# Performance work log

Measured on AMD Instinct MI355X. Metric: run time of the kernel, lower is better.

## Reference

```python
import jax, jax.numpy as jnp
import numpy as np

N_NODES = 10000
N_EDGES = 200000
NODE_DIM = 128
EDGE_DIM = 16
CONV_DIM = 64
HEADS = 5
NEG_SLOPE = 0.2


def gatv2_layer(x, src, dst, edge_attr, Wl, bl, We, att, bias):
    # PyG GATv2Conv, share_weights=True, concat=False, add_self_loops=True, eval mode
    N = x.shape[0]
    H, C = att.shape
    xl = (x @ Wl + bl).reshape(N, H, C)  # [N,H,C]; x_r = x_l (share_weights)
    # self loops, edge_attr fill_value='mean' (mean of incoming edge_attr per node)
    deg = jax.ops.segment_sum(jnp.ones(dst.shape[0], x.dtype), dst, num_segments=N)
    loop_attr = jax.ops.segment_sum(edge_attr, dst, num_segments=N) / jnp.maximum(deg, 1.0)[:, None]
    loop = jnp.arange(N, dtype=src.dtype)
    src_f = jnp.concatenate([src, loop])
    dst_f = jnp.concatenate([dst, loop])
    ea = jnp.concatenate([edge_attr, loop_attr], axis=0)
    e_emb = (ea @ We).reshape(-1, H, C)  # [E+N,H,C]
    m = jax.nn.leaky_relu(xl[src_f] + xl[dst_f] + e_emb, NEG_SLOPE)
    score = jnp.einsum('ehc,hc->eh', m, att)  # [E+N,H]
    # per-destination softmax over incoming edges
    smax = jax.ops.segment_max(score, dst_f, num_segments=N)
    ex = jnp.exp(score - smax[dst_f])
    denom = jax.ops.segment_sum(ex, dst_f, num_segments=N)
    alpha = ex / denom[dst_f]
    out = jax.ops.segment_sum(alpha[:, :, None] * xl[src_f], dst_f, num_segments=N)
    return out.mean(axis=1) + bias  # concat=False -> mean over heads


def setup_inputs() -> dict:
    key = jax.random.key(0)
    ks = jax.random.split(key, 32)
    inp = {
        'x': jax.random.normal(ks[0], (N_NODES, NODE_DIM), jnp.float32),
        'edge_index': jax.random.randint(ks[1], (2, N_EDGES), 0, N_NODES, dtype=jnp.int32),
        'edge_attr': jax.random.normal(ks[2], (N_EDGES, EDGE_DIM), jnp.float32),
    }
    in_dims = [NODE_DIM, CONV_DIM, CONV_DIM]
    HC = HEADS * CONV_DIM
    k = 3
    for l in range(3):
        d = in_dims[l]
        inp[f'Wl{l}'] = jax.random.normal(ks[k], (d, HC), jnp.float32) / np.float32(np.sqrt(d)); k += 1
        inp[f'bl{l}'] = jnp.zeros((HC,), jnp.float32)
        inp[f'We{l}'] = jax.random.normal(ks[k], (EDGE_DIM, HC), jnp.float32) / np.float32(np.sqrt(EDGE_DIM)); k += 1
        inp[f'att{l}'] = jax.random.normal(ks[k], (HEADS, CONV_DIM), jnp.float32) / np.float32(np.sqrt(CONV_DIM)); k += 1
        inp[f'b{l}'] = jnp.zeros((CONV_DIM,), jnp.float32)
    return inp


def reference(x, edge_index, edge_attr,
              Wl0, bl0, We0, att0, b0,
              Wl1, bl1, We1, att1, b1,
              Wl2, bl2, We2, att2, b2):
    src, dst = edge_index[0], edge_index[1]
    h = x
    layers = [(Wl0, bl0, We0, att0, b0), (Wl1, bl1, We1, att1, b1), (Wl2, bl2, We2, att2, b2)]
    for Wl, bl, We, att, b in layers:
        h = gatv2_layer(h, src, dst, edge_attr, Wl, bl, We, att, b)
        h = jax.nn.elu(h)
    return h
```

## Files before the change

### kernel.cpp

```cpp
#include <hip/hip_runtime.h>
#include <hip/hip_bf16.h>


#define NN 10000
#define NE 200000
#define ND 128
#define ED 16
#define CD 64
#define NH 5
#define HC 320
#define EF 210000
#define EFP 210048
#define NEG 0.2f
#define SB 103

__global__ void k_count(const int* __restrict__ dst, int* __restrict__ deg) {
  int e = blockIdx.x * blockDim.x + threadIdx.x;
  if (e >= NE) return;
  atomicAdd(&deg[dst[e]], 1);
}

__global__ __launch_bounds__(1024) void k_scan(const int* __restrict__ deg,
                                               int* __restrict__ rowptr) {
  __shared__ int part[1024];
  int t = threadIdx.x;
  int base = t * 10;
  int local[10];
  int s = 0;
  #pragma unroll
  for (int j = 0; j < 10; j++) {
    int i = base + j;
    local[j] = (i < NN) ? deg[i] : 0;
    s += local[j];
  }
  part[t] = s;
  __syncthreads();
  for (int off = 1; off < 1024; off <<= 1) {
    int v = (t >= off) ? part[t - off] : 0;
    __syncthreads();
    part[t] += v;
    __syncthreads();
  }
  int prefix = (t > 0) ? part[t - 1] : 0;
  #pragma unroll
  for (int j = 0; j < 10; j++) {
    int i = base + j;
    if (i < NN) rowptr[i] = prefix;
    prefix += local[j];
  }
  if (t == 1023) rowptr[NN] = prefix;
}

__global__ void k_fill(const int* __restrict__ ei, const int* __restrict__ rowptr,
                       int* __restrict__ cursor, int* __restrict__ csr_eid,
                       int* __restrict__ csr_src, int* __restrict__ csr_dst) {
  int e = blockIdx.x * blockDim.x + threadIdx.x;
  if (e >= NE) return;
  int d = ei[NE + e];
  int slot = atomicAdd(&cursor[d], 1);
  int pos = rowptr[d] + slot;
  csr_eid[pos] = e;
  csr_src[pos] = ei[e];
  csr_dst[pos] = d;
}

__global__ __launch_bounds__(256) void k_loopattr(const int* __restrict__ csr_eid,
                                                  const int* __restrict__ rowptr,
                                                  const float* __restrict__ eattr,
                                                  float* __restrict__ loop_attr) {
  int wave = threadIdx.x >> 6, lane = threadIdx.x & 63;
  int d = blockIdx.x * 4 + wave;
  if (d >= NN) return;
  int g = lane >> 4, k = lane & 15;
  int b = rowptr[d], n = rowptr[d + 1] - b;
  float s = 0.f;
  for (int i = g; i < n; i += 4)
    s += eattr[(size_t)csr_eid[b + i] * ED + k];
  s += __shfl_xor(s, 16, 64);
  s += __shfl_xor(s, 32, 64);
  if (g == 0) loop_attr[d * ED + k] = s / fmaxf((float)n, 1.0f);
}

__global__ void k_eacsr(const int* __restrict__ csr_eid, const float* __restrict__ eattr,
                        float* __restrict__ ea_csr) {
  int idx = blockIdx.x * blockDim.x + threadIdx.x;
  if (idx >= NE * 4) return;
  int p = idx >> 2, q = idx & 3;
  const float4* sp = (const float4*)(eattr + (size_t)csr_eid[p] * ED);
  ((float4*)(ea_csr + (size_t)p * ED))[q] = sp[q];
}

__global__ void k_wet(const float* __restrict__ We, float* __restrict__ WeT) {
  int i = blockIdx.x * blockDim.x + threadIdx.x;
  if (i >= ED * HC) return;
  int hc = i >> 4, k = i & 15;
  WeT[i] = We[k * HC + hc];
}

template <int D>
__global__ __launch_bounds__(320) void k_xl(const float* __restrict__ h,
                                            const float* __restrict__ Wl,
                                            const float* __restrict__ bl,
                                            float* __restrict__ xl) {
  constexpr int NPB = 8;
  int node0 = blockIdx.x * NPB;
  int t = threadIdx.x;
  float acc[NPB];
  #pragma unroll
  for (int i = 0; i < NPB; i++) acc[i] = 0.f;
  for (int k = 0; k < D; k += 4) {
    float w0 = Wl[(k + 0) * HC + t];
    float w1 = Wl[(k + 1) * HC + t];
    float w2 = Wl[(k + 2) * HC + t];
    float w3 = Wl[(k + 3) * HC + t];
    #pragma unroll
    for (int i = 0; i < NPB; i++) {
      float4 hv = *(const float4*)(h + (size_t)(node0 + i) * D + k);
      acc[i] += hv.x * w0 + hv.y * w1 + hv.z * w2 + hv.w * w3;
    }
  }
  float bv = bl[t];
  #pragma unroll
  for (int i = 0; i < NPB; i++)
    xl[(size_t)(node0 + i) * HC + t] = acc[i] + bv;
}

__device__ __forceinline__ float dot4(float4 a, float4 b) {
  return a.x * b.x + a.y * b.y + a.z * b.z + a.w * b.w;
}

__global__ __launch_bounds__(256) void k_score(
    const int* __restrict__ csr_src, const int* __restrict__ csr_dst,
    const float* __restrict__ ea_csr, const float* __restrict__ loop_attr,
    const float* __restrict__ xl, const float* __restrict__ WeT,
    const float* __restrict__ att, float* __restrict__ wP) {
  int bid = blockIdx.x;
  int lb = (bid & 7) * SB + (bid >> 3);
  int p = lb * 256 + threadIdx.x;
  if (p >= EF) return;
  int h = blockIdx.y;
  int s, d;
  const float* ea;
  if (p < NE) { s = csr_src[p]; d = csr_dst[p]; ea = ea_csr + (size_t)p * ED; }
  else        { s = d = p - NE; ea = loop_attr + (size_t)(p - NE) * ED; }
  float4 ea4[4];
  {
    const float4* q = (const float4*)ea;
    ea4[0] = q[0]; ea4[1] = q[1]; ea4[2] = q[2]; ea4[3] = q[3];
  }
  const float* xsrow = xl + (size_t)s * HC + h * CD;
  const float* xdrow = xl + (size_t)d * HC + h * CD;
  const float* wrow  = WeT + h * CD * ED;
  const float* arow  = att + h * CD;
  float sc = 0.f;
  #pragma unroll 4
  for (int cb = 0; cb < CD; cb += 4) {
    float4 xs4 = *(const float4*)(xsrow + cb);
    float4 xd4 = *(const float4*)(xdrow + cb);
    const float4* w0 = (const float4*)(wrow + (cb + 0) * ED);
    const float4* w1 = (const float4*)(wrow + (cb + 1) * ED);
    const float4* w2 = (const float4*)(wrow + (cb + 2) * ED);
    const float4* w3 = (const float4*)(wrow + (cb + 3) * ED);
    float z0 = xs4.x + xd4.x + dot4(ea4[0], w0[0]) + dot4(ea4[1], w0[1]) +
               dot4(ea4[2], w0[2]) + dot4(ea4[3], w0[3]);
    float z1 = xs4.y + xd4.y + dot4(ea4[0], w1[0]) + dot4(ea4[1], w1[1]) +
               dot4(ea4[2], w1[2]) + dot4(ea4[3], w1[3]);
    float z2 = xs4.z + xd4.z + dot4(ea4[0], w2[0]) + dot4(ea4[1], w2[1]) +
               dot4(ea4[2], w2[2]) + dot4(ea4[3], w2[3]);
    float z3 = xs4.w + xd4.w + dot4(ea4[0], w3[0]) + dot4(ea4[1], w3[1]) +
               dot4(ea4[2], w3[2]) + dot4(ea4[3], w3[3]);
    z0 *= (z0 > 0.f) ? 1.0f : NEG;
    z1 *= (z1 > 0.f) ? 1.0f : NEG;
    z2 *= (z2 > 0.f) ? 1.0f : NEG;
    z3 *= (z3 > 0.f) ? 1.0f : NEG;
    float4 a4 = *(const float4*)(arow + cb);
    sc += a4.x * z0 + a4.y * z1 + a4.z * z2 + a4.w * z3;
  }
  sc = fminf(fmaxf(sc, -60.f), 60.f);
  wP[(size_t)h * EFP + p] = __expf(sc);
}

__global__ __launch_bounds__(320) void k_agg(
    const int* __restrict__ csr_src, const int* __restrict__ rowptr,
    const float* __restrict__ wP, const float* __restrict__ xl,
    const float* __restrict__ bias, float* __restrict__ out) {
  __shared__ float s_v[NH][CD];
  int h = threadIdx.x >> 6, lane = threadIdx.x & 63;
  int d = blockIdx.x;
  int b = rowptr[d], n = rowptr[d + 1] - b;
  const float* sp = wP + (size_t)h * EFP;
  const float* xlh = xl + h * CD + lane;
  float dn = sp[NE + d];
  float acc = dn * xlh[(size_t)d * HC];
  int p = b, pe = b + n;
  for (; p + 4 <= pe; p += 4) {
    int s0 = csr_src[p], s1 = csr_src[p + 1], s2 = csr_src[p + 2], s3 = csr_src[p + 3];
    float w0 = sp[p], w1 = sp[p + 1], w2 = sp[p + 2], w3 = sp[p + 3];
    float x0 = xlh[(size_t)s0 * HC];
    float x1 = xlh[(size_t)s1 * HC];
    float x2 = xlh[(size_t)s2 * HC];
    float x3 = xlh[(size_t)s3 * HC];
    dn += (w0 + w1) + (w2 + w3);
    acc += w0 * x0 + w1 * x1 + w2 * x2 + w3 * x3;
  }
  for (; p < pe; p++) {
    int s0 = csr_src[p];
    float w0 = sp[p];
    dn += w0;
    acc += w0 * xlh[(size_t)s0 * HC];
  }
  s_v[h][lane] = acc / dn;
  __syncthreads();
  if (h == 0) {
    float v = s_v[0][lane] + s_v[1][lane] + s_v[2][lane] + s_v[3][lane] + s_v[4][lane];
    v = v * (1.0f / NH) + bias[lane];
    v = v > 0.f ? v : expm1f(v);
    out[(size_t)d * CD + lane] = v;
  }
}

extern "C" void kernel_launch(void* const* d_in, const int* in_sizes, int n_in,
                              void* d_out, int out_size, void* d_ws, size_t ws_size,
                              hipStream_t stream) {
  const float* x = (const float*)d_in[0];
  const int* ei = (const int*)d_in[1];
  const float* eattr = (const float*)d_in[2];

  char* w = (char*)d_ws;
  int* degi      = (int*)w;                 w += NN * 4;
  int* cursor    = (int*)w;                 w += NN * 4;
  int* rowptr    = (int*)w;                 w += (NN + 1) * 4;
  int* csr_eid   = (int*)w;                 w += NE * 4;
  int* csr_src   = (int*)w;                 w += NE * 4;
  int* csr_dst   = (int*)w;                 w += NE * 4;
  float* loop_attr = (float*)w;             w += (size_t)NN * ED * 4;
  float* ea_csr  = (float*)w;               w += (size_t)NE * ED * 4;
  float* xl      = (float*)w;               w += (size_t)NN * HC * 4;
  float* wPbuf   = (float*)w;               w += (size_t)NH * EFP * 4;
  float* WeT     = (float*)w;               w += (size_t)ED * HC * 4;
  float* hbuf    = (float*)w;               w += (size_t)NN * CD * 4;

  hipMemsetAsync(degi, 0, NN * 4, stream);
  hipMemsetAsync(cursor, 0, NN * 4, stream);
  k_count<<<(NE + 255) / 256, 256, 0, stream>>>(ei + NE, degi);
  k_scan<<<1, 1024, 0, stream>>>(degi, rowptr);
  k_fill<<<(NE + 255) / 256, 256, 0, stream>>>(ei, rowptr, cursor, csr_eid, csr_src, csr_dst);
  k_loopattr<<<(NN + 3) / 4, 256, 0, stream>>>(csr_eid, rowptr, eattr, loop_attr);
  k_eacsr<<<(NE * 4 + 255) / 256, 256, 0, stream>>>(csr_eid, eattr, ea_csr);

  for (int l = 0; l < 3; l++) {
    const float* Wl  = (const float*)d_in[3 + 5 * l];
    const float* bl  = (const float*)d_in[4 + 5 * l];
    const float* We  = (const float*)d_in[5 + 5 * l];
    const float* att = (const float*)d_in[6 + 5 * l];
    const float* b   = (const float*)d_in[7 + 5 * l];

    k_wet<<<(ED * HC + 255) / 256, 256, 0, stream>>>(We, WeT);
    if (l == 0) k_xl<ND><<<NN / 8, 320, 0, stream>>>(x, Wl, bl, xl);
    else        k_xl<CD><<<NN / 8, 320, 0, stream>>>(hbuf, Wl, bl, xl);

    dim3 gs(8 * SB, NH);
    k_score<<<gs, 256, 0, stream>>>(csr_src, csr_dst, ea_csr, loop_attr,
                                    xl, WeT, att, wPbuf);

    float* dst_out = (l < 2) ? hbuf : (float*)d_out;
    k_agg<<<NN, 320, 0, stream>>>(csr_src, rowptr, wPbuf, xl, b, dst_out);
  }
}
```

Measured before the change: 526.3 us.

## Store projected features head-major and flatten score grid with XCD-aware swizzle

The projected node features are now stored head-major ([H][N][C]) instead of node-major, so each head's rows form a compact 2.56 MB slab. The score kernel drops the 2D grid and uses a flat 1D grid, remapped so that each group of consecutive blocks (one per XCD) covers a contiguous range of head/edge tiles. Together these aim to keep the gather working set for each head within one XCD's L2. This adds index arithmetic and relies on the constants PB, TOTB and PERX matching the edge count and head count exactly.

```diff
diff --git a/kernel.cpp b/kernel.cpp
--- a/kernel.cpp
+++ b/kernel.cpp
@@ -12,7 +12,9 @@
 #define EF 210000
 #define EFP 210048
 #define NEG 0.2f
-#define SB 103
+#define PB 824
+#define TOTB 4120
+#define PERX 515
 
 __global__ void k_count(const int* __restrict__ dst, int* __restrict__ deg) {
   int e = blockIdx.x * blockDim.x + threadIdx.x;
@@ -120,9 +122,10 @@
     }
   }
   float bv = bl[t];
+  int hh = t >> 6, c = t & 63;
   #pragma unroll
   for (int i = 0; i < NPB; i++)
-    xl[(size_t)(node0 + i) * HC + t] = acc[i] + bv;
+    xl[((size_t)hh * NN + node0 + i) * CD + c] = acc[i] + bv;
 }
 
 __device__ __forceinline__ float dot4(float4 a, float4 b) {
@@ -135,10 +138,11 @@
     const float* __restrict__ xl, const float* __restrict__ WeT,
     const float* __restrict__ att, float* __restrict__ wP) {
   int bid = blockIdx.x;
-  int lb = (bid & 7) * SB + (bid >> 3);
+  int w = (bid & 7) * PERX + (bid >> 3);
+  int h = w / PB;
+  int lb = w - h * PB;
   int p = lb * 256 + threadIdx.x;
   if (p >= EF) return;
-  int h = blockIdx.y;
   int s, d;
   const float* ea;
   if (p < NE) { s = csr_src[p]; d = csr_dst[p]; ea = ea_csr + (size_t)p * ED; }
@@ -148,8 +152,8 @@
     const float4* q = (const float4*)ea;
     ea4[0] = q[0]; ea4[1] = q[1]; ea4[2] = q[2]; ea4[3] = q[3];
   }
-  const float* xsrow = xl + (size_t)s * HC + h * CD;
-  const float* xdrow = xl + (size_t)d * HC + h * CD;
+  const float* xsrow = xl + ((size_t)h * NN + s) * CD;
+  const float* xdrow = xl + ((size_t)h * NN + d) * CD;
   const float* wrow  = WeT + h * CD * ED;
   const float* arow  = att + h * CD;
   float sc = 0.f;
@@ -189,17 +193,17 @@
   int d = blockIdx.x;
   int b = rowptr[d], n = rowptr[d + 1] - b;
   const float* sp = wP + (size_t)h * EFP;
-  const float* xlh = xl + h * CD + lane;
+  const float* xlh = xl + (size_t)h * NN * CD + lane;
   float dn = sp[NE + d];
-  float acc = dn * xlh[(size_t)d * HC];
+  float acc = dn * xlh[(size_t)d * CD];
   int p = b, pe = b + n;
   for (; p + 4 <= pe; p += 4) {
     int s0 = csr_src[p], s1 = csr_src[p + 1], s2 = csr_src[p + 2], s3 = csr_src[p + 3];
     float w0 = sp[p], w1 = sp[p + 1], w2 = sp[p + 2], w3 = sp[p + 3];
-    float x0 = xlh[(size_t)s0 * HC];
-    float x1 = xlh[(size_t)s1 * HC];
-    float x2 = xlh[(size_t)s2 * HC];
-    float x3 = xlh[(size_t)s3 * HC];
+    float x0 = xlh[(size_t)s0 * CD];
+    float x1 = xlh[(size_t)s1 * CD];
+    float x2 = xlh[(size_t)s2 * CD];
+    float x3 = xlh[(size_t)s3 * CD];
     dn += (w0 + w1) + (w2 + w3);
     acc += w0 * x0 + w1 * x1 + w2 * x2 + w3 * x3;
   }
@@ -207,7 +211,7 @@
     int s0 = csr_src[p];
     float w0 = sp[p];
     dn += w0;
-    acc += w0 * xlh[(size_t)s0 * HC];
+    acc += w0 * xlh[(size_t)s0 * CD];
   }
   s_v[h][lane] = acc / dn;
   __syncthreads();
@@ -259,9 +263,8 @@
     if (l == 0) k_xl<ND><<<NN / 8, 320, 0, stream>>>(x, Wl, bl, xl);
     else        k_xl<CD><<<NN / 8, 320, 0, stream>>>(hbuf, Wl, bl, xl);
 
-    dim3 gs(8 * SB, NH);
-    k_score<<<gs, 256, 0, stream>>>(csr_src, csr_dst, ea_csr, loop_attr,
-                                    xl, WeT, att, wPbuf);
+    k_score<<<TOTB, 256, 0, stream>>>(csr_src, csr_dst, ea_csr, loop_attr,
+                                      xl, WeT, att, wPbuf);
 
     float* dst_out = (l < 2) ? hbuf : (float*)d_out;
     k_agg<<<NN, 320, 0, stream>>>(csr_src, rowptr, wPbuf, xl, b, dst_out);
```

Measured after the change: 522.9 us. About the same (-0.6%).
